# Kernel optimization log

Measured on AMD Instinct MI355X. Metric: run time of the kernel, lower is better.

Reference implementation:

```python
import jax, jax.numpy as jnp
import numpy as np

N_FILTER = 32
NCENTS = 1024
BETA = 0.25  # commitment cost


def setup_inputs() -> dict:
    key = jax.random.key(0)
    k1, k2 = jax.random.split(key)
    lat = jax.random.normal(k1, (2048, 2048), dtype=jnp.float32)
    centroids = jax.random.normal(k2, (NCENTS, N_FILTER), dtype=jnp.float32)
    leak_factor = jnp.ones((), dtype=jnp.float32)
    return {"lat": lat, "centroids": centroids, "leak_factor": leak_factor}


def _vq(z, centroids):
    # z: [B, L, D]; centroids: [K, D]
    zf = z.reshape(-1, z.shape[-1])  # [N, D]
    # squared distances: ||z||^2 - 2 z.c + ||c||^2  -> [N, K]
    d = (jnp.sum(zf * zf, axis=1, keepdims=True)
         - 2.0 * zf @ centroids.T
         + jnp.sum(centroids * centroids, axis=1)[None, :])
    idx = jnp.argmin(d, axis=1)  # [N]
    zq = centroids[idx]  # gather, [N, D]
    sg = jax.lax.stop_gradient
    # VQ-VAE codebook + commitment losses
    loss = jnp.mean((sg(zf) - zq) ** 2) + BETA * jnp.mean((zf - sg(zq)) ** 2)
    # straight-through estimator
    zq_st = zf + sg(zq - zf)
    return zq_st.reshape(z.shape), loss


def reference(lat, centroids, leak_factor):
    B = lat.shape[0]
    lat_size = lat.shape[1]
    z = lat.reshape(B, lat_size // N_FILTER, N_FILTER)
    _zq, cent_loss = _vq(z, centroids)
    # NOTE: original forward overwrites the quantized result with raw lat
    new_lat = lat.reshape(B, lat_size)
    lf = jnp.clip(leak_factor, 0.001, 1000.0)
    return new_lat * lf, cent_loss
```

## Files before the change

### kernel.cpp

```cpp
#include <hip/hip_runtime.h>

#define D 32
#define K 1024
#define N_ROWS 131072
#define TOTAL_ELEMS 4194304
#define LOSS_SCALE (1.25f / 4194304.0f)
#define BIAS 192.0f

typedef __attribute__((ext_vector_type(8))) short short8;
typedef __attribute__((ext_vector_type(4))) float f32x4;

__device__ __forceinline__ unsigned short f2bf(float f) {
  unsigned u = __builtin_bit_cast(unsigned, f);
  unsigned r = u + 0x7FFFu + ((u >> 16) & 1u);
  return (unsigned short)(r >> 16);
}

__global__ __launch_bounds__(256) void prep_kernel(
    const float* __restrict__ cent, unsigned short* __restrict__ centbf,
    float* __restrict__ cnormb, float* __restrict__ loss_out) {
  int t = blockIdx.x * 256 + threadIdx.x;
  centbf[t] = f2bf(-2.0f * cent[t]);
  if (t == 0) *loss_out = 0.0f;
  if (t < K) {
    const float* c = cent + t * D;
    float s0 = 0.f, s1 = 0.f, s2 = 0.f, s3 = 0.f;
#pragma unroll
    for (int d = 0; d < D; d += 4) {
      s0 = fmaf(c[d], c[d], s0);
      s1 = fmaf(c[d + 1], c[d + 1], s1);
      s2 = fmaf(c[d + 2], c[d + 2], s2);
      s3 = fmaf(c[d + 3], c[d + 3], s3);
    }
    cnormb[t] = (s0 + s1) + (s2 + s3) + BIAS;
  }
}

__global__ __launch_bounds__(256) void vq_kernel(
    const float* __restrict__ lat, const float* __restrict__ cent,
    const unsigned short* __restrict__ centbf, const float* __restrict__ cnormb,
    const float* __restrict__ lf_ptr, float* __restrict__ out,
    float* __restrict__ loss_out) {
  __shared__ short8 sB8[2048];
  __shared__ float sCn[512];
  __shared__ float wsum[4];
  const int tid = threadIdx.x;
  const int lane = tid & 63;
  const int wave = tid >> 6;
  const int quad = lane >> 4;
  const int col  = lane & 15;
  const int rowbase = blockIdx.x * 128 + wave * 32;

  float lf = fminf(fmaxf(lf_ptr[0], 0.001f), 1000.0f);
  short8 a0, a1;
  {
    const float* p0 = lat + (size_t)(rowbase + col) * D + quad * 8;
    const float* p1 = p0 + 16 * D;
    float4 u0 = ((const float4*)p0)[0], u1 = ((const float4*)p0)[1];
    float4 w0 = ((const float4*)p1)[0], w1 = ((const float4*)p1)[1];
    a0[0] = (short)f2bf(u0.x); a0[1] = (short)f2bf(u0.y);
    a0[2] = (short)f2bf(u0.z); a0[3] = (short)f2bf(u0.w);
    a0[4] = (short)f2bf(u1.x); a0[5] = (short)f2bf(u1.y);
    a0[6] = (short)f2bf(u1.z); a0[7] = (short)f2bf(u1.w);
    a1[0] = (short)f2bf(w0.x); a1[1] = (short)f2bf(w0.y);
    a1[2] = (short)f2bf(w0.z); a1[3] = (short)f2bf(w0.w);
    a1[4] = (short)f2bf(w1.x); a1[5] = (short)f2bf(w1.y);
    a1[6] = (short)f2bf(w1.z); a1[7] = (short)f2bf(w1.w);
    float* o0 = out + (size_t)(rowbase + col) * D + quad * 8;
    float* o1 = o0 + 16 * D;
    float4 s00 = {u0.x * lf, u0.y * lf, u0.z * lf, u0.w * lf};
    float4 s01 = {u1.x * lf, u1.y * lf, u1.z * lf, u1.w * lf};
    float4 s10 = {w0.x * lf, w0.y * lf, w0.z * lf, w0.w * lf};
    float4 s11 = {w1.x * lf, w1.y * lf, w1.z * lf, w1.w * lf};
    ((float4*)o0)[0] = s00;
    ((float4*)o0)[1] = s01;
    ((float4*)o1)[0] = s10;
    ((float4*)o1)[1] = s11;
  }

  const f32x4 zero = {0.f, 0.f, 0.f, 0.f};
  unsigned pk0[4] = {0xFFFFFFFFu, 0xFFFFFFFFu, 0xFFFFFFFFu, 0xFFFFFFFFu};
  unsigned pk1[4] = {0xFFFFFFFFu, 0xFFFFFFFFu, 0xFFFFFFFFu, 0xFFFFFFFFu};

  const short8* gB8 = (const short8*)centbf;

  for (int p = 0; p < 2; ++p) {
    __syncthreads();
#pragma unroll
    for (int j = 0; j < 8; ++j)
      sB8[j * 256 + tid] = gB8[p * 2048 + j * 256 + tid];
    sCn[tid] = cnormb[p * 512 + tid];
    sCn[tid + 256] = cnormb[p * 512 + 256 + tid];
    __syncthreads();

#pragma unroll 8
    for (int f = 0; f < 32; ++f) {
      short8 b = sB8[f * 64 + col * 4 + quad];
      float cn = sCn[f * 16 + col];
      f32x4 d0 = __builtin_amdgcn_mfma_f32_16x16x32_bf16(a0, b, zero, 0, 0, 0);
      f32x4 d1 = __builtin_amdgcn_mfma_f32_16x16x32_bf16(a1, b, zero, 0, 0, 0);
      const unsigned idxv = (unsigned)(p * 512 + f * 16 + col);
#pragma unroll
      for (int r = 0; r < 4; ++r) {
        float s0 = d0[r] + cn;
        unsigned q0 = (__builtin_bit_cast(unsigned, s0) & 0xFFFFFC00u) | idxv;
        pk0[r] = pk0[r] < q0 ? pk0[r] : q0;
        float s1 = d1[r] + cn;
        unsigned q1 = (__builtin_bit_cast(unsigned, s1) & 0xFFFFFC00u) | idxv;
        pk1[r] = pk1[r] < q1 ? pk1[r] : q1;
      }
    }
  }

#pragma unroll
  for (int off = 1; off < 16; off <<= 1) {
#pragma unroll
    for (int r = 0; r < 4; ++r) {
      unsigned o0 = __shfl_xor(pk0[r], off);
      pk0[r] = pk0[r] < o0 ? pk0[r] : o0;
      unsigned o1 = __shfl_xor(pk1[r], off);
      pk1[r] = pk1[r] < o1 ? pk1[r] : o1;
    }
  }

  const int rsel = lane & 3;
  const int q = (lane >> 2) & 3;
  float s = 0.f;
#pragma unroll
  for (int t = 0; t < 2; ++t) {
    unsigned pk = (t == 0) ? pk0[rsel] : pk1[rsel];
    int row = rowbase + t * 16 + quad * 4 + rsel;
    int ci = (int)(pk & 1023u);
    const float* zp = lat + (size_t)row * D + q * 8;
    const float* cp = cent + (size_t)ci * D + q * 8;
    float4 za = ((const float4*)zp)[0], zb = ((const float4*)zp)[1];
    float4 ca = ((const float4*)cp)[0], cb = ((const float4*)cp)[1];
    float f0 = za.x - ca.x, f1 = za.y - ca.y, f2 = za.z - ca.z, f3 = za.w - ca.w;
    float g0 = zb.x - cb.x, g1 = zb.y - cb.y, g2 = zb.z - cb.z, g3 = zb.w - cb.w;
    float m0 = fmaf(f0, f0, g0 * g0);
    float m1 = fmaf(f1, f1, g1 * g1);
    float m2 = fmaf(f2, f2, g2 * g2);
    float m3 = fmaf(f3, f3, g3 * g3);
    s += (m0 + m1) + (m2 + m3);
  }
  s += __shfl_xor(s, 4);
  s += __shfl_xor(s, 8);
  s += __shfl_xor(s, 1);
  s += __shfl_xor(s, 2);
  s += __shfl_xor(s, 16);
  s += __shfl_xor(s, 32);

  if (lane == 0) wsum[wave] = s;
  __syncthreads();
  if (threadIdx.x == 0) {
    float blk = (wsum[0] + wsum[1]) + (wsum[2] + wsum[3]);
    atomicAdd(loss_out, blk * LOSS_SCALE);
  }
}

extern "C" void kernel_launch(void* const* d_in, const int* in_sizes, int n_in,
                              void* d_out, int out_size, void* d_ws, size_t ws_size,
                              hipStream_t stream) {
  const float* lat  = (const float*)d_in[0];
  const float* cent = (const float*)d_in[1];
  const float* lf   = (const float*)d_in[2];
  float* out = (float*)d_out;
  unsigned short* centbf = (unsigned short*)d_ws;
  float* cnormb = (float*)((char*)d_ws + K * D * sizeof(unsigned short));
  float* loss = out + TOTAL_ELEMS;

  prep_kernel<<<K * D / 256, 256, 0, stream>>>(cent, centbf, cnormb, loss);
  vq_kernel<<<N_ROWS / 128, 256, 0, stream>>>(lat, cent, centbf, cnormb, lf,
                                              out, loss);
}
```

Baseline: 98.14 us.

## Load full codebook once per block and process two row tiles per block

```diff
diff --git a/kernel.cpp b/kernel.cpp
--- a/kernel.cpp
+++ b/kernel.cpp
@@ -41,31 +41,40 @@
     const unsigned short* __restrict__ centbf, const float* __restrict__ cnormb,
     const float* __restrict__ lf_ptr, float* __restrict__ out,
     float* __restrict__ loss_out) {
-  __shared__ short8 sB8[2048];
-  __shared__ float sCn[512];
+  __shared__ short8 sB8[4096];
+  __shared__ float sCn[1024];
   __shared__ float wsum[4];
   const int tid = threadIdx.x;
   const int lane = tid & 63;
   const int wave = tid >> 6;
   const int quad = lane >> 4;
   const int col  = lane & 15;
-  const int rowbase = blockIdx.x * 128 + wave * 32;
+
+  {
+    const short8* gB8 = (const short8*)centbf;
+#pragma unroll
+    for (int j = 0; j < 16; ++j) sB8[j * 256 + tid] = gB8[j * 256 + tid];
+#pragma unroll
+    for (int j = 0; j < 4; ++j) sCn[j * 256 + tid] = cnormb[j * 256 + tid];
+  }
 
   float lf = fminf(fmaxf(lf_ptr[0], 0.001f), 1000.0f);
-  short8 a0, a1;
-  {
+  short8 a[2][2];
+#pragma unroll
+  for (int it = 0; it < 2; ++it) {
+    const int rowbase = blockIdx.x * 256 + it * 128 + wave * 32;
     const float* p0 = lat + (size_t)(rowbase + col) * D + quad * 8;
     const float* p1 = p0 + 16 * D;
     float4 u0 = ((const float4*)p0)[0], u1 = ((const float4*)p0)[1];
     float4 w0 = ((const float4*)p1)[0], w1 = ((const float4*)p1)[1];
-    a0[0] = (short)f2bf(u0.x); a0[1] = (short)f2bf(u0.y);
-    a0[2] = (short)f2bf(u0.z); a0[3] = (short)f2bf(u0.w);
-    a0[4] = (short)f2bf(u1.x); a0[5] = (short)f2bf(u1.y);
-    a0[6] = (short)f2bf(u1.z); a0[7] = (short)f2bf(u1.w);
-    a1[0] = (short)f2bf(w0.x); a1[1] = (short)f2bf(w0.y);
-    a1[2] = (short)f2bf(w0.z); a1[3] = (short)f2bf(w0.w);
-    a1[4] = (short)f2bf(w1.x); a1[5] = (short)f2bf(w1.y);
-    a1[6] = (short)f2bf(w1.z); a1[7] = (short)f2bf(w1.w);
+    a[it][0][0] = (short)f2bf(u0.x); a[it][0][1] = (short)f2bf(u0.y);
+    a[it][0][2] = (short)f2bf(u0.z); a[it][0][3] = (short)f2bf(u0.w);
+    a[it][0][4] = (short)f2bf(u1.x); a[it][0][5] = (short)f2bf(u1.y);
+    a[it][0][6] = (short)f2bf(u1.z); a[it][0][7] = (short)f2bf(u1.w);
+    a[it][1][0] = (short)f2bf(w0.x); a[it][1][1] = (short)f2bf(w0.y);
+    a[it][1][2] = (short)f2bf(w0.z); a[it][1][3] = (short)f2bf(w0.w);
+    a[it][1][4] = (short)f2bf(w1.x); a[it][1][5] = (short)f2bf(w1.y);
+    a[it][1][6] = (short)f2bf(w1.z); a[it][1][7] = (short)f2bf(w1.w);
     float* o0 = out + (size_t)(rowbase + col) * D + quad * 8;
     float* o1 = o0 + 16 * D;
     float4 s00 = {u0.x * lf, u0.y * lf, u0.z * lf, u0.w * lf};
@@ -77,29 +86,25 @@
     ((float4*)o1)[0] = s10;
     ((float4*)o1)[1] = s11;
   }
+  __syncthreads();
 
   const f32x4 zero = {0.f, 0.f, 0.f, 0.f};
-  unsigned pk0[4] = {0xFFFFFFFFu, 0xFFFFFFFFu, 0xFFFFFFFFu, 0xFFFFFFFFu};
-  unsigned pk1[4] = {0xFFFFFFFFu, 0xFFFFFFFFu, 0xFFFFFFFFu, 0xFFFFFFFFu};
+  float sacc = 0.f;
 
-  const short8* gB8 = (const short8*)centbf;
-
-  for (int p = 0; p < 2; ++p) {
-    __syncthreads();
 #pragma unroll
-    for (int j = 0; j < 8; ++j)
-      sB8[j * 256 + tid] = gB8[p * 2048 + j * 256 + tid];
-    sCn[tid] = cnormb[p * 512 + tid];
-    sCn[tid + 256] = cnormb[p * 512 + 256 + tid];
-    __syncthreads();
+  for (int it = 0; it < 2; ++it) {
+    const int rowbase = blockIdx.x * 256 + it * 128 + wave * 32;
+    const short8 a0 = a[it][0], a1 = a[it][1];
+    unsigned pk0[4] = {0xFFFFFFFFu, 0xFFFFFFFFu, 0xFFFFFFFFu, 0xFFFFFFFFu};
+    unsigned pk1[4] = {0xFFFFFFFFu, 0xFFFFFFFFu, 0xFFFFFFFFu, 0xFFFFFFFFu};
 
 #pragma unroll 8
-    for (int f = 0; f < 32; ++f) {
+    for (int f = 0; f < 64; ++f) {
       short8 b = sB8[f * 64 + col * 4 + quad];
       float cn = sCn[f * 16 + col];
       f32x4 d0 = __builtin_amdgcn_mfma_f32_16x16x32_bf16(a0, b, zero, 0, 0, 0);
       f32x4 d1 = __builtin_amdgcn_mfma_f32_16x16x32_bf16(a1, b, zero, 0, 0, 0);
-      const unsigned idxv = (unsigned)(p * 512 + f * 16 + col);
+      const unsigned idxv = (unsigned)(f * 16 + col);
 #pragma unroll
       for (int r = 0; r < 4; ++r) {
         float s0 = d0[r] + cn;
@@ -110,47 +115,50 @@
         pk1[r] = pk1[r] < q1 ? pk1[r] : q1;
       }
     }
+
+#pragma unroll
+    for (int off = 1; off < 16; off <<= 1) {
+#pragma unroll
+      for (int r = 0; r < 4; ++r) {
+        unsigned o0 = __shfl_xor(pk0[r], off);
+        pk0[r] = pk0[r] < o0 ? pk0[r] : o0;
+        unsigned o1 = __shfl_xor(pk1[r], off);
+        pk1[r] = pk1[r] < o1 ? pk1[r] : o1;
+      }
+    }
+
+    const int rsel = lane & 3;
+    const int q = (lane >> 2) & 3;
+    float s = 0.f;
+#pragma unroll
+    for (int t = 0; t < 2; ++t) {
+      unsigned pk = (t == 0) ? pk0[rsel] : pk1[rsel];
+      int row = rowbase + t * 16 + quad * 4 + rsel;
+      int ci = (int)(pk & 1023u);
+      const float* zp = lat + (size_t)row * D + q * 8;
+      const float* cp = cent + (size_t)ci * D + q * 8;
+      float4 za = ((const float4*)zp)[0], zb = ((const float4*)zp)[1];
+      float4 ca = ((const float4*)cp)[0], cb = ((const float4*)cp)[1];
+      float f0 = za.x - ca.x, f1 = za.y - ca.y;
+      float f2 = za.z - ca.z, f3 = za.w - ca.w;
+      float g0 = zb.x - cb.x, g1 = zb.y - cb.y;
+      float g2 = zb.z - cb.z, g3 = zb.w - cb.w;
+      float m0 = fmaf(f0, f0, g0 * g0);
+      float m1 = fmaf(f1, f1, g1 * g1);
+      float m2 = fmaf(f2, f2, g2 * g2);
+      float m3 = fmaf(f3, f3, g3 * g3);
+      s += (m0 + m1) + (m2 + m3);
+    }
+    s += __shfl_xor(s, 4);
+    s += __shfl_xor(s, 8);
+    s += __shfl_xor(s, 1);
+    s += __shfl_xor(s, 2);
+    s += __shfl_xor(s, 16);
+    s += __shfl_xor(s, 32);
+    sacc += s;
   }
 
-#pragma unroll
-  for (int off = 1; off < 16; off <<= 1) {
-#pragma unroll
-    for (int r = 0; r < 4; ++r) {
-      unsigned o0 = __shfl_xor(pk0[r], off);
-      pk0[r] = pk0[r] < o0 ? pk0[r] : o0;
-      unsigned o1 = __shfl_xor(pk1[r], off);
-      pk1[r] = pk1[r] < o1 ? pk1[r] : o1;
-    }
-  }
-
-  const int rsel = lane & 3;
-  const int q = (lane >> 2) & 3;
-  float s = 0.f;
-#pragma unroll
-  for (int t = 0; t < 2; ++t) {
-    unsigned pk = (t == 0) ? pk0[rsel] : pk1[rsel];
-    int row = rowbase + t * 16 + quad * 4 + rsel;
-    int ci = (int)(pk & 1023u);
-    const float* zp = lat + (size_t)row * D + q * 8;
-    const float* cp = cent + (size_t)ci * D + q * 8;
-    float4 za = ((const float4*)zp)[0], zb = ((const float4*)zp)[1];
-    float4 ca = ((const float4*)cp)[0], cb = ((const float4*)cp)[1];
-    float f0 = za.x - ca.x, f1 = za.y - ca.y, f2 = za.z - ca.z, f3 = za.w - ca.w;
-    float g0 = zb.x - cb.x, g1 = zb.y - cb.y, g2 = zb.z - cb.z, g3 = zb.w - cb.w;
-    float m0 = fmaf(f0, f0, g0 * g0);
-    float m1 = fmaf(f1, f1, g1 * g1);
-    float m2 = fmaf(f2, f2, g2 * g2);
-    float m3 = fmaf(f3, f3, g3 * g3);
-    s += (m0 + m1) + (m2 + m3);
-  }
-  s += __shfl_xor(s, 4);
-  s += __shfl_xor(s, 8);
-  s += __shfl_xor(s, 1);
-  s += __shfl_xor(s, 2);
-  s += __shfl_xor(s, 16);
-  s += __shfl_xor(s, 32);
-
-  if (lane == 0) wsum[wave] = s;
+  if (lane == 0) wsum[wave] = sacc;
   __syncthreads();
   if (threadIdx.x == 0) {
     float blk = (wsum[0] + wsum[1]) + (wsum[2] + wsum[3]);
@@ -170,6 +178,6 @@
   float* loss = out + TOTAL_ELEMS;
 
   prep_kernel<<<K * D / 256, 256, 0, stream>>>(cent, centbf, cnormb, loss);
-  vq_kernel<<<N_ROWS / 128, 256, 0, stream>>>(lat, cent, centbf, cnormb, lf,
+  vq_kernel<<<N_ROWS / 256, 256, 0, stream>>>(lat, cent, centbf, cnormb, lf,
                                               out, loss);
 }
```

Result: no change. 97.68 us (-0.5%).

## Split codebook search across two blocks per row tile and add combine kernel

Applied to the files above, without the earlier changes.

```diff
diff --git a/kernel.cpp b/kernel.cpp
--- a/kernel.cpp
+++ b/kernel.cpp
@@ -36,20 +36,28 @@
   }
 }
 
-__global__ __launch_bounds__(256) void vq_kernel(
-    const float* __restrict__ lat, const float* __restrict__ cent,
-    const unsigned short* __restrict__ centbf, const float* __restrict__ cnormb,
-    const float* __restrict__ lf_ptr, float* __restrict__ out,
-    float* __restrict__ loss_out) {
+__global__ __launch_bounds__(256) void vq_main(
+    const float* __restrict__ lat, const unsigned short* __restrict__ centbf,
+    const float* __restrict__ cnormb, const float* __restrict__ lf_ptr,
+    float* __restrict__ out, unsigned* __restrict__ wswin) {
   __shared__ short8 sB8[2048];
   __shared__ float sCn[512];
-  __shared__ float wsum[4];
   const int tid = threadIdx.x;
   const int lane = tid & 63;
   const int wave = tid >> 6;
   const int quad = lane >> 4;
   const int col  = lane & 15;
-  const int rowbase = blockIdx.x * 128 + wave * 32;
+  const int half = blockIdx.x & 1;
+  const int rowbase = (blockIdx.x >> 1) * 128 + wave * 32;
+
+  {
+    const short8* gB8 = (const short8*)centbf;
+#pragma unroll
+    for (int j = 0; j < 8; ++j)
+      sB8[j * 256 + tid] = gB8[half * 2048 + j * 256 + tid];
+    sCn[tid] = cnormb[half * 512 + tid];
+    sCn[256 + tid] = cnormb[half * 512 + 256 + tid];
+  }
 
   float lf = fminf(fmaxf(lf_ptr[0], 0.001f), 1000.0f);
   short8 a0, a1;
@@ -66,49 +74,40 @@
     a1[2] = (short)f2bf(w0.z); a1[3] = (short)f2bf(w0.w);
     a1[4] = (short)f2bf(w1.x); a1[5] = (short)f2bf(w1.y);
     a1[6] = (short)f2bf(w1.z); a1[7] = (short)f2bf(w1.w);
-    float* o0 = out + (size_t)(rowbase + col) * D + quad * 8;
-    float* o1 = o0 + 16 * D;
-    float4 s00 = {u0.x * lf, u0.y * lf, u0.z * lf, u0.w * lf};
-    float4 s01 = {u1.x * lf, u1.y * lf, u1.z * lf, u1.w * lf};
-    float4 s10 = {w0.x * lf, w0.y * lf, w0.z * lf, w0.w * lf};
-    float4 s11 = {w1.x * lf, w1.y * lf, w1.z * lf, w1.w * lf};
-    ((float4*)o0)[0] = s00;
-    ((float4*)o0)[1] = s01;
-    ((float4*)o1)[0] = s10;
-    ((float4*)o1)[1] = s11;
+    if (half == 0) {
+      float* o0 = out + (size_t)(rowbase + col) * D + quad * 8;
+      float* o1 = o0 + 16 * D;
+      float4 s00 = {u0.x * lf, u0.y * lf, u0.z * lf, u0.w * lf};
+      float4 s01 = {u1.x * lf, u1.y * lf, u1.z * lf, u1.w * lf};
+      float4 s10 = {w0.x * lf, w0.y * lf, w0.z * lf, w0.w * lf};
+      float4 s11 = {w1.x * lf, w1.y * lf, w1.z * lf, w1.w * lf};
+      ((float4*)o0)[0] = s00;
+      ((float4*)o0)[1] = s01;
+      ((float4*)o1)[0] = s10;
+      ((float4*)o1)[1] = s11;
+    }
   }
+  __syncthreads();
 
   const f32x4 zero = {0.f, 0.f, 0.f, 0.f};
   unsigned pk0[4] = {0xFFFFFFFFu, 0xFFFFFFFFu, 0xFFFFFFFFu, 0xFFFFFFFFu};
   unsigned pk1[4] = {0xFFFFFFFFu, 0xFFFFFFFFu, 0xFFFFFFFFu, 0xFFFFFFFFu};
 
-  const short8* gB8 = (const short8*)centbf;
-
-  for (int p = 0; p < 2; ++p) {
-    __syncthreads();
+#pragma unroll 8
+  for (int f = 0; f < 32; ++f) {
+    short8 b = sB8[f * 64 + col * 4 + quad];
+    float cn = sCn[f * 16 + col];
+    f32x4 d0 = __builtin_amdgcn_mfma_f32_16x16x32_bf16(a0, b, zero, 0, 0, 0);
+    f32x4 d1 = __builtin_amdgcn_mfma_f32_16x16x32_bf16(a1, b, zero, 0, 0, 0);
+    const unsigned idxv = (unsigned)(half * 512 + f * 16 + col);
 #pragma unroll
-    for (int j = 0; j < 8; ++j)
-      sB8[j * 256 + tid] = gB8[p * 2048 + j * 256 + tid];
-    sCn[tid] = cnormb[p * 512 + tid];
-    sCn[tid + 256] = cnormb[p * 512 + 256 + tid];
-    __syncthreads();
-
-#pragma unroll 8
-    for (int f = 0; f < 32; ++f) {
-      short8 b = sB8[f * 64 + col * 4 + quad];
-      float cn = sCn[f * 16 + col];
-      f32x4 d0 = __builtin_amdgcn_mfma_f32_16x16x32_bf16(a0, b, zero, 0, 0, 0);
-      f32x4 d1 = __builtin_amdgcn_mfma_f32_16x16x32_bf16(a1, b, zero, 0, 0, 0);
-      const unsigned idxv = (unsigned)(p * 512 + f * 16 + col);
-#pragma unroll
-      for (int r = 0; r < 4; ++r) {
-        float s0 = d0[r] + cn;
-        unsigned q0 = (__builtin_bit_cast(unsigned, s0) & 0xFFFFFC00u) | idxv;
-        pk0[r] = pk0[r] < q0 ? pk0[r] : q0;
-        float s1 = d1[r] + cn;
-        unsigned q1 = (__builtin_bit_cast(unsigned, s1) & 0xFFFFFC00u) | idxv;
-        pk1[r] = pk1[r] < q1 ? pk1[r] : q1;
-      }
+    for (int r = 0; r < 4; ++r) {
+      float s0 = d0[r] + cn;
+      unsigned q0 = (__builtin_bit_cast(unsigned, s0) & 0xFFFFFC00u) | idxv;
+      pk0[r] = pk0[r] < q0 ? pk0[r] : q0;
+      float s1 = d1[r] + cn;
+      unsigned q1 = (__builtin_bit_cast(unsigned, s1) & 0xFFFFFC00u) | idxv;
+      pk1[r] = pk1[r] < q1 ? pk1[r] : q1;
     }
   }
 
@@ -125,36 +124,49 @@
 
   const int rsel = lane & 3;
   const int q = (lane >> 2) & 3;
-  float s = 0.f;
+  if (q == 0) {
 #pragma unroll
-  for (int t = 0; t < 2; ++t) {
-    unsigned pk = (t == 0) ? pk0[rsel] : pk1[rsel];
-    int row = rowbase + t * 16 + quad * 4 + rsel;
-    int ci = (int)(pk & 1023u);
-    const float* zp = lat + (size_t)row * D + q * 8;
-    const float* cp = cent + (size_t)ci * D + q * 8;
-    float4 za = ((const float4*)zp)[0], zb = ((const float4*)zp)[1];
-    float4 ca = ((const float4*)cp)[0], cb = ((const float4*)cp)[1];
-    float f0 = za.x - ca.x, f1 = za.y - ca.y, f2 = za.z - ca.z, f3 = za.w - ca.w;
-    float g0 = zb.x - cb.x, g1 = zb.y - cb.y, g2 = zb.z - cb.z, g3 = zb.w - cb.w;
-    float m0 = fmaf(f0, f0, g0 * g0);
-    float m1 = fmaf(f1, f1, g1 * g1);
-    float m2 = fmaf(f2, f2, g2 * g2);
-    float m3 = fmaf(f3, f3, g3 * g3);
-    s += (m0 + m1) + (m2 + m3);
+    for (int t = 0; t < 2; ++t) {
+      unsigned pk = (t == 0) ? pk0[rsel] : pk1[rsel];
+      int row = rowbase + t * 16 + quad * 4 + rsel;
+      wswin[half * N_ROWS + row] = pk;
+    }
   }
-  s += __shfl_xor(s, 4);
-  s += __shfl_xor(s, 8);
-  s += __shfl_xor(s, 1);
-  s += __shfl_xor(s, 2);
-  s += __shfl_xor(s, 16);
-  s += __shfl_xor(s, 32);
+}
 
-  if (lane == 0) wsum[wave] = s;
+__global__ __launch_bounds__(256) void combine_kernel(
+    const float* __restrict__ lat, const float* __restrict__ cent,
+    const unsigned* __restrict__ wswin, float* __restrict__ loss_out) {
+  const int row = blockIdx.x * 256 + threadIdx.x;
+  unsigned u0 = wswin[row];
+  unsigned u1 = wswin[N_ROWS + row];
+  unsigned u = u0 < u1 ? u0 : u1;
+  int ci = (int)(u & 1023u);
+
+  const float4* zp = (const float4*)(lat + (size_t)row * D);
+  const float4* cp = (const float4*)(cent + (size_t)ci * D);
+  float m0 = 0.f, m1 = 0.f, m2 = 0.f, m3 = 0.f;
+#pragma unroll
+  for (int i = 0; i < 8; ++i) {
+    float4 z4 = zp[i], c4 = cp[i];
+    float f0 = z4.x - c4.x, f1 = z4.y - c4.y;
+    float f2 = z4.z - c4.z, f3 = z4.w - c4.w;
+    m0 = fmaf(f0, f0, m0); m1 = fmaf(f1, f1, m1);
+    m2 = fmaf(f2, f2, m2); m3 = fmaf(f3, f3, m3);
+  }
+  float dmin = (m0 + m1) + (m2 + m3);
+
+#pragma unroll
+  for (int off = 32; off > 0; off >>= 1) dmin += __shfl_down(dmin, off);
+
+  __shared__ float wsum[4];
+  const int lane = threadIdx.x & 63;
+  const int wave = threadIdx.x >> 6;
+  if (lane == 0) wsum[wave] = dmin;
   __syncthreads();
   if (threadIdx.x == 0) {
-    float blk = (wsum[0] + wsum[1]) + (wsum[2] + wsum[3]);
-    atomicAdd(loss_out, blk * LOSS_SCALE);
+    float s = (wsum[0] + wsum[1]) + (wsum[2] + wsum[3]);
+    atomicAdd(loss_out, s * LOSS_SCALE);
   }
 }
 
@@ -166,10 +178,11 @@
   const float* lf   = (const float*)d_in[2];
   float* out = (float*)d_out;
   unsigned short* centbf = (unsigned short*)d_ws;
-  float* cnormb = (float*)((char*)d_ws + K * D * sizeof(unsigned short));
+  float* cnormb = (float*)((char*)d_ws + 65536);
+  unsigned* wswin = (unsigned*)((char*)d_ws + 65536 + 4096);
   float* loss = out + TOTAL_ELEMS;
 
   prep_kernel<<<K * D / 256, 256, 0, stream>>>(cent, centbf, cnormb, loss);
-  vq_kernel<<<N_ROWS / 128, 256, 0, stream>>>(lat, cent, centbf, cnormb, lf,
-                                              out, loss);
+  vq_main<<<2048, 256, 0, stream>>>(lat, centbf, cnormb, lf, out, wswin);
+  combine_kernel<<<N_ROWS / 256, 256, 0, stream>>>(lat, cent, wswin, loss);
 }
```

New measurement: 107.0 us. +9.0%, slower.

## Load whole codebook once per 512-thread block and software-pipeline MFMA loop

Applied to the files above, without the earlier changes.

```diff
diff --git a/kernel.cpp b/kernel.cpp
--- a/kernel.cpp
+++ b/kernel.cpp
@@ -36,20 +36,28 @@
   }
 }
 
-__global__ __launch_bounds__(256) void vq_kernel(
+__global__ __launch_bounds__(512) void vq_kernel(
     const float* __restrict__ lat, const float* __restrict__ cent,
     const unsigned short* __restrict__ centbf, const float* __restrict__ cnormb,
     const float* __restrict__ lf_ptr, float* __restrict__ out,
     float* __restrict__ loss_out) {
-  __shared__ short8 sB8[2048];
-  __shared__ float sCn[512];
-  __shared__ float wsum[4];
+  __shared__ short8 sB8[4096];
+  __shared__ float sCn[1024];
+  __shared__ float wsum[8];
   const int tid = threadIdx.x;
   const int lane = tid & 63;
   const int wave = tid >> 6;
   const int quad = lane >> 4;
   const int col  = lane & 15;
-  const int rowbase = blockIdx.x * 128 + wave * 32;
+  const int rowbase = blockIdx.x * 256 + wave * 32;
+
+  {
+    const short8* gB8 = (const short8*)centbf;
+#pragma unroll
+    for (int j = 0; j < 8; ++j) sB8[j * 512 + tid] = gB8[j * 512 + tid];
+    sCn[tid] = cnormb[tid];
+    sCn[512 + tid] = cnormb[512 + tid];
+  }
 
   float lf = fminf(fmaxf(lf_ptr[0], 0.001f), 1000.0f);
   short8 a0, a1;
@@ -77,38 +85,47 @@
     ((float4*)o1)[0] = s10;
     ((float4*)o1)[1] = s11;
   }
+  __syncthreads();
 
   const f32x4 zero = {0.f, 0.f, 0.f, 0.f};
   unsigned pk0[4] = {0xFFFFFFFFu, 0xFFFFFFFFu, 0xFFFFFFFFu, 0xFFFFFFFFu};
   unsigned pk1[4] = {0xFFFFFFFFu, 0xFFFFFFFFu, 0xFFFFFFFFu, 0xFFFFFFFFu};
 
-  const short8* gB8 = (const short8*)centbf;
+  const int boff = col * 4 + quad;
 
-  for (int p = 0; p < 2; ++p) {
-    __syncthreads();
+  short8 b = sB8[boff];
+  float cn = sCn[col];
+  f32x4 d0 = __builtin_amdgcn_mfma_f32_16x16x32_bf16(a0, b, zero, 0, 0, 0);
+  f32x4 d1 = __builtin_amdgcn_mfma_f32_16x16x32_bf16(a1, b, zero, 0, 0, 0);
+
+#pragma unroll 7
+  for (int f = 1; f < 64; ++f) {
+    short8 bn = sB8[f * 64 + boff];
+    float cnn = sCn[f * 16 + col];
+    f32x4 e0 = __builtin_amdgcn_mfma_f32_16x16x32_bf16(a0, bn, zero, 0, 0, 0);
+    f32x4 e1 = __builtin_amdgcn_mfma_f32_16x16x32_bf16(a1, bn, zero, 0, 0, 0);
+    const unsigned idxv = (unsigned)(((f - 1) << 4) | col);
 #pragma unroll
-    for (int j = 0; j < 8; ++j)
-      sB8[j * 256 + tid] = gB8[p * 2048 + j * 256 + tid];
-    sCn[tid] = cnormb[p * 512 + tid];
-    sCn[tid + 256] = cnormb[p * 512 + 256 + tid];
-    __syncthreads();
-
-#pragma unroll 8
-    for (int f = 0; f < 32; ++f) {
-      short8 b = sB8[f * 64 + col * 4 + quad];
-      float cn = sCn[f * 16 + col];
-      f32x4 d0 = __builtin_amdgcn_mfma_f32_16x16x32_bf16(a0, b, zero, 0, 0, 0);
-      f32x4 d1 = __builtin_amdgcn_mfma_f32_16x16x32_bf16(a1, b, zero, 0, 0, 0);
-      const unsigned idxv = (unsigned)(p * 512 + f * 16 + col);
+    for (int r = 0; r < 4; ++r) {
+      float s0 = d0[r] + cn;
+      unsigned q0 = (__builtin_bit_cast(unsigned, s0) & 0xFFFFFC00u) | idxv;
+      pk0[r] = min(pk0[r], q0);
+      float s1 = d1[r] + cn;
+      unsigned q1 = (__builtin_bit_cast(unsigned, s1) & 0xFFFFFC00u) | idxv;
+      pk1[r] = min(pk1[r], q1);
+    }
+    d0 = e0; d1 = e1; cn = cnn;
+  }
+  {
+    const unsigned idxv = (unsigned)((63 << 4) | col);
 #pragma unroll
-      for (int r = 0; r < 4; ++r) {
-        float s0 = d0[r] + cn;
-        unsigned q0 = (__builtin_bit_cast(unsigned, s0) & 0xFFFFFC00u) | idxv;
-        pk0[r] = pk0[r] < q0 ? pk0[r] : q0;
-        float s1 = d1[r] + cn;
-        unsigned q1 = (__builtin_bit_cast(unsigned, s1) & 0xFFFFFC00u) | idxv;
-        pk1[r] = pk1[r] < q1 ? pk1[r] : q1;
-      }
+    for (int r = 0; r < 4; ++r) {
+      float s0 = d0[r] + cn;
+      unsigned q0 = (__builtin_bit_cast(unsigned, s0) & 0xFFFFFC00u) | idxv;
+      pk0[r] = min(pk0[r], q0);
+      float s1 = d1[r] + cn;
+      unsigned q1 = (__builtin_bit_cast(unsigned, s1) & 0xFFFFFC00u) | idxv;
+      pk1[r] = min(pk1[r], q1);
     }
   }
 
@@ -117,9 +134,9 @@
 #pragma unroll
     for (int r = 0; r < 4; ++r) {
       unsigned o0 = __shfl_xor(pk0[r], off);
-      pk0[r] = pk0[r] < o0 ? pk0[r] : o0;
+      pk0[r] = min(pk0[r], o0);
       unsigned o1 = __shfl_xor(pk1[r], off);
-      pk1[r] = pk1[r] < o1 ? pk1[r] : o1;
+      pk1[r] = min(pk1[r], o1);
     }
   }
 
@@ -152,8 +169,9 @@
 
   if (lane == 0) wsum[wave] = s;
   __syncthreads();
-  if (threadIdx.x == 0) {
-    float blk = (wsum[0] + wsum[1]) + (wsum[2] + wsum[3]);
+  if (tid == 0) {
+    float blk = ((wsum[0] + wsum[1]) + (wsum[2] + wsum[3])) +
+                ((wsum[4] + wsum[5]) + (wsum[6] + wsum[7]));
     atomicAdd(loss_out, blk * LOSS_SCALE);
   }
 }
@@ -170,6 +188,6 @@
   float* loss = out + TOTAL_ELEMS;
 
   prep_kernel<<<K * D / 256, 256, 0, stream>>>(cent, centbf, cnormb, loss);
-  vq_kernel<<<N_ROWS / 128, 256, 0, stream>>>(lat, cent, centbf, cnormb, lf,
+  vq_kernel<<<N_ROWS / 256, 512, 0, stream>>>(lat, cent, centbf, cnormb, lf,
                                               out, loss);
 }
```

Result: no change. 96.60 us (-1.6%).
